# Optimization experiments

Measured on AMD Instinct MI355X. Metric: run time of the kernel, lower is better.

## Reference

```python
import jax, jax.numpy as jnp
import numpy as np

D = 4096       # embed_dim
H = 16         # num_heads
HD = D // H    # head_dim = 256
MLP_H = int(D * 2.0)  # 8192
L_V = 2048
L_T = 1024
GAMMA = 0.6
NOISE_STD = 0.07
TEMP = 0.05
LN_EPS = 1e-5


def setup_inputs() -> dict:
    key = jax.random.key(0)
    ks = jax.random.split(key, 16)
    s = 0.02
    return {
        "vision_feature": jax.random.normal(ks[0], (L_V, D), jnp.float32),
        "text_embed": jax.random.normal(ks[1], (L_T, D), jnp.float32),
        "attention_mask": jnp.zeros((L_T,), jnp.float32),  # additive mask, 0 = attend
        "noise": jax.random.normal(ks[2], (L_V,), jnp.float32),
        "Wq": jax.random.normal(ks[3], (D, D), jnp.float32) * s,
        "bq": jnp.zeros((D,), jnp.float32),
        "Wk": jax.random.normal(ks[4], (D, D), jnp.float32) * s,
        "bk": jnp.zeros((D,), jnp.float32),
        "Wv": jax.random.normal(ks[5], (D, D), jnp.float32) * s,
        "bv": jnp.zeros((D,), jnp.float32),
        "Wo": jax.random.normal(ks[6], (D, D), jnp.float32) * s,
        "bo": jnp.zeros((D,), jnp.float32),
        "ln_w": jnp.ones((D,), jnp.float32),
        "ln_b": jnp.zeros((D,), jnp.float32),
        "W1": jax.random.normal(ks[7], (MLP_H, D), jnp.float32) * s,
        "b1": jnp.zeros((MLP_H,), jnp.float32),
        "W2": jax.random.normal(ks[8], (1, MLP_H), jnp.float32) * s,
        "b2": jnp.zeros((1,), jnp.float32),
    }


def reference(vision_feature, text_embed, attention_mask, noise,
              Wq, bq, Wk, bk, Wv, bv, Wo, bo, ln_w, ln_b, W1, b1, W2, b2):
    # --- cross attention (vision queries over text keys/values) ---
    q = (vision_feature @ Wq.T + bq).reshape(L_V, H, HD)
    k = (text_embed @ Wk.T + bk).reshape(L_T, H, HD)
    v = (text_embed @ Wv.T + bv).reshape(L_T, H, HD)
    logits = jnp.einsum('qhd,khd->hqk', q, k) / np.float32(np.sqrt(HD))
    logits = logits + attention_mask[None, None, :]  # additive attn_mask
    attn = jax.nn.softmax(logits, axis=-1)
    ctx = jnp.einsum('hqk,khd->qhd', attn, v).reshape(L_V, D)
    attn_out = ctx @ Wo.T + bo
    # --- residual + layernorm ---
    x = vision_feature + attn_out
    mu = jnp.mean(x, axis=-1, keepdims=True)
    var = jnp.mean(jnp.square(x - mu), axis=-1, keepdims=True)
    xn = (x - mu) / jnp.sqrt(var + LN_EPS) * ln_w + ln_b
    # --- tiny MLP scorer ---
    h = jax.nn.gelu(xn @ W1.T + b1, approximate=False)
    weight_scores = (h @ W2.T + b2)[:, 0] + noise * NOISE_STD
    # --- temperature softmax over all tokens, top-p (gamma) selection ---
    p = jax.nn.softmax(weight_scores / TEMP, axis=0)
    order = jnp.argsort(-p)           # descending sort indices
    cum = jnp.cumsum(p[order])
    keep = cum <= GAMMA               # threshold_index prefix mask
    gathered = vision_feature[order]  # [L_V, D]
    # fixed-shape stand-in for indices[:threshold_index] gather:
    # valid selected rows are the nonzero prefix
    return jnp.where(keep[:, None], gathered, jnp.zeros((), gathered.dtype))
```

## Files before the change

### kernel.cpp

```cpp
#include <hip/hip_runtime.h>
#include <math.h>


#define LV   2048
#define LT   1024
#define DIM  4096
#define NHD  16
#define HDD  256
#define MLPH 8192

typedef __attribute__((ext_vector_type(8))) short bfx8;
typedef __attribute__((ext_vector_type(4))) float fx4;
typedef unsigned short u16;

__device__ __forceinline__ float wave_sum(float v){
#pragma unroll
  for (int o = 32; o > 0; o >>= 1) v += __shfl_xor(v, o);
  return v;
}
__device__ __forceinline__ float wave_max(float v){
#pragma unroll
  for (int o = 32; o > 0; o >>= 1) v = fmaxf(v, __shfl_xor(v, o));
  return v;
}

__device__ __forceinline__ void splitpack(const float4 a, const float4 b,
                                          bfx8* hi, bfx8* lo){
  float f[8] = {a.x,a.y,a.z,a.w, b.x,b.y,b.z,b.w};
  union { bfx8 v; unsigned u[4]; } H, L;
#pragma unroll
  for (int p = 0; p < 4; ++p){
    unsigned u0 = __float_as_uint(f[2*p]);
    unsigned u1 = __float_as_uint(f[2*p+1]);
    H.u[p] = (u0 >> 16) | (u1 & 0xffff0000u);
    float h0 = __uint_as_float(u0 & 0xffff0000u);
    float h1 = __uint_as_float(u1 & 0xffff0000u);
    unsigned v0 = __float_as_uint(f[2*p]   - h0);
    unsigned v1 = __float_as_uint(f[2*p+1] - h1);
    L.u[p] = (v0 >> 16) | (v1 & 0xffff0000u);
  }
  *hi = H.v; *lo = L.v;
}

__device__ __forceinline__ void split1(float v, u16* h, u16* l){
  unsigned uv = __float_as_uint(v);
  *h = (u16)(uv >> 16);
  float hf = __uint_as_float(uv & 0xffff0000u);
  *l = (u16)(__float_as_uint(v - hf) >> 16);
}

__device__ __forceinline__ void glds16(const void* g, void* l){
  __builtin_amdgcn_global_load_lds(
      (const __attribute__((address_space(1))) unsigned int*)g,
      (__attribute__((address_space(3))) unsigned int*)l, 16, 0, 0);
}

__global__ __launch_bounds__(256)
void repack_kernel(const float* __restrict__ src, u16* __restrict__ hi,
                   u16* __restrict__ lo, int Kc, int ktsh)
{
  const long long e = ((long long)blockIdx.x * 256 + threadIdx.x) * 8;
  const int T = (int)(e >> 9);
  const int L = (int)(e >> 3) & 63;
  const int rt = T >> ktsh, kt = T & ((1 << ktsh) - 1);
  const int r = (rt << 4) + (L & 15);
  const int k = (kt << 5) + ((L >> 4) << 3);
  const float* p = src + (long long)r * Kc + k;
  bfx8 h, l;
  splitpack(*(const float4*)p, *(const float4*)(p + 4), &h, &l);
  *(bfx8*)(hi + e) = h;
  *(bfx8*)(lo + e) = l;
}

template<int MODE>
__global__ __launch_bounds__(256)
void mgemm(const u16* __restrict__ Ah, const u16* __restrict__ Al, int aKT, long long aZe,
           const u16* __restrict__ Bh, const u16* __restrict__ Bl, int bKT, long long bZe,
           float* __restrict__ C, int ldc, long long cZe,
           u16* __restrict__ XH, u16* __restrict__ XL, int cKT, int coff0, int czoff,
           const float* __restrict__ w2, float* __restrict__ part, int nbase,
           const float* __restrict__ bias,
           int nx, int KT, int kt0, int zkt, float alpha)
{
  __shared__ bfx8 lbuf[2][32][64];
  __shared__ float parts[2][128];
  const int tid  = threadIdx.x;
  const int lane = tid & 63;
  const int wv   = tid >> 6;
  const int wr   = wv >> 1, wc = wv & 1;
  const int nwg  = gridDim.x;
  const int id   = blockIdx.x;
  int bm, bn;
  {
    const int my = nwg / nx;
    if (((nx & 3) == 0) && ((my & 1) == 0) && ((nwg & 7) == 0)){
      const int rm = my >> 1, rn = nx >> 2;
      const int x  = id & 7;
      const int j  = id >> 3;
      bm = ((x >> 2) * rm) + j / rn;
      bn = ((x & 3) * rn) + j % rn;
    } else if (((my & 7) == 0) && ((nwg & 7) == 0)){
      const int rm = my >> 3;
      const int x = id & 7, j = id >> 3;
      bm = x * rm + j / nx;
      bn = j % nx;
    } else { bm = id / nx; bn = id % nx; }
  }
  const int m0 = bm << 7;
  const int n0 = bn << 7;
  const int z    = blockIdx.z;
  const u16* Ahz = Ah + (long long)z * aZe;
  const u16* Alz = Al + (long long)z * aZe;
  const u16* Bhz = Bh + (long long)z * bZe;
  const u16* Blz = Bl + (long long)z * bZe;
  C += (long long)z * cZe;
  const int coff = coff0 + z * czoff;
  const int ktb  = kt0 + z * zkt;
  const int rtA0 = m0 >> 4, rtB0 = n0 >> 4;

  const fx4 zz = {0.f, 0.f, 0.f, 0.f};
  fx4 acc[4][4];
#pragma unroll
  for (int i = 0; i < 4; ++i)
#pragma unroll
    for (int j = 0; j < 4; ++j) acc[i][j] = zz;

  const u16* wbase = (wv == 0) ? Ahz : (wv == 1) ? Alz : (wv == 2) ? Bhz : Blz;
  const int  wrt0  = (wv < 2) ? rtA0 : rtB0;
  const int  wKT   = (wv < 2) ? aKT  : bKT;

#define STAGE(BUF, KTI)                                                        \
  {                                                                            \
    _Pragma("unroll")                                                          \
    for (int q = 0; q < 8; ++q){                                               \
      const u16* g = wbase + ((long long)(wrt0 + q) * wKT + (KTI)) * 512       \
                     + lane * 8;                                               \
      glds16((const void*)g, (void*)&lbuf[BUF][wv * 8 + q][0]);                \
    }                                                                          \
  }

#define KSTEP(WAITASM, DOSTAGE)                                                \
  {                                                                            \
    asm volatile(WAITASM ::: "memory");                                        \
    __builtin_amdgcn_sched_barrier(0);                                         \
    __builtin_amdgcn_s_barrier();                                              \
    __builtin_amdgcn_sched_barrier(0);                                         \
    bfx8 ah[4], al[4], bh[4], bl[4];                                           \
    _Pragma("unroll")                                                          \
    for (int i = 0; i < 4; ++i){                                               \
      ah[i] = lbuf[cur][     wr*4 + i][lane];                                  \
      al[i] = lbuf[cur][ 8 + wr*4 + i][lane];                                  \
      bh[i] = lbuf[cur][16 + wc*4 + i][lane];                                  \
      bl[i] = lbuf[cur][24 + wc*4 + i][lane];                                  \
    }                                                                          \
    asm volatile("s_waitcnt lgkmcnt(0)" ::: "memory");                         \
    __builtin_amdgcn_sched_barrier(0);                                         \
    __builtin_amdgcn_s_barrier();                                              \
    __builtin_amdgcn_sched_barrier(0);                                         \
    if (DOSTAGE) STAGE(cur, ktb + t + 2);                                      \
    __builtin_amdgcn_sched_barrier(0);                                         \
    _Pragma("unroll")                                                          \
    for (int i = 0; i < 4; ++i)                                                \
      _Pragma("unroll")                                                        \
      for (int j = 0; j < 4; ++j){                                             \
        acc[i][j] = __builtin_amdgcn_mfma_f32_16x16x32_bf16(ah[i], bl[j], acc[i][j], 0, 0, 0); \
        acc[i][j] = __builtin_amdgcn_mfma_f32_16x16x32_bf16(al[i], bh[j], acc[i][j], 0, 0, 0); \
        acc[i][j] = __builtin_amdgcn_mfma_f32_16x16x32_bf16(ah[i], bh[j], acc[i][j], 0, 0, 0); \
      }                                                                        \
    cur ^= 1;                                                                  \
  }

  STAGE(0, ktb);
  STAGE(1, ktb + 1);
  int cur = 0;
  for (int t = 0; t < KT - 1; ++t)
    KSTEP("s_waitcnt vmcnt(8)", (t + 2 < KT));
  { const int t = KT - 1; (void)t; KSTEP("s_waitcnt vmcnt(0)", 0); }
#undef KSTEP
#undef STAGE

  if (MODE == 0){
#pragma unroll
    for (int i = 0; i < 4; ++i){
      const int row0 = m0 + wr*64 + i*16 + ((lane >> 4) << 2);
#pragma unroll
      for (int j = 0; j < 4; ++j){
        const int col = n0 + wc*64 + j*16 + (lane & 15);
        const float bb = bias ? bias[col] : 0.0f;
#pragma unroll
        for (int r = 0; r < 4; ++r)
          C[(size_t)(row0 + r)*ldc + col] = alpha*acc[i][j][r] + bb;
      }
    }
  } else if (MODE == 2){
#pragma unroll
    for (int i = 0; i < 4; ++i){
      const int row0 = m0 + wr*64 + i*16 + ((lane >> 4) << 2);
#pragma unroll
      for (int j = 0; j < 4; ++j){
        const int ncol = n0 + wc*64 + j*16 + (lane & 15);
        const int colg = coff + ncol;
        const float bb = bias ? bias[ncol] : 0.0f;
        const long long base = (long long)(row0 >> 4) * cKT + (colg >> 5);
        const int el = colg & 7;
        const int sl0 = ((colg >> 3) & 3) * 16 + (row0 & 15);
        u16* ph = XH + base*512 + el;
        u16* pl = XL + base*512 + el;
#pragma unroll
        for (int r = 0; r < 4; ++r){
          u16 hh, llo;
          split1(alpha*acc[i][j][r] + bb, &hh, &llo);
          ph[(sl0 + r)*8] = hh;
          pl[(sl0 + r)*8] = llo;
        }
      }
    }
  } else if (MODE == 3){
#pragma unroll
    for (int i = 0; i < 4; ++i){
      const int row0 = m0 + wr*64 + i*16 + ((lane >> 4) << 2);
#pragma unroll
      for (int j = 0; j < 4; ++j){
        const int d = n0 + wc*64 + j*16 + (lane & 15);
        const float bb = bias ? bias[d] : 0.0f;
        short4 hs, ls;
        u16 h0,l0,h1,l1,h2,l2,h3,l3;
        split1(alpha*acc[i][j][0] + bb, &h0, &l0);
        split1(alpha*acc[i][j][1] + bb, &h1, &l1);
        split1(alpha*acc[i][j][2] + bb, &h2, &l2);
        split1(alpha*acc[i][j][3] + bb, &h3, &l3);
        hs.x=(short)h0; hs.y=(short)h1; hs.z=(short)h2; hs.w=(short)h3;
        ls.x=(short)l0; ls.y=(short)l1; ls.z=(short)l2; ls.w=(short)l3;
        const long long T = (long long)(d >> 4) * cKT + (row0 >> 5);
        const int sl = ((row0 >> 3) & 3) * 16 + (d & 15);
        *(short4*)(XH + T*512 + sl*8 + (row0 & 7)) = hs;
        *(short4*)(XL + T*512 + sl*8 + (row0 & 7)) = ls;
      }
    }
  } else if (MODE == 4){
    float rp[16];
#pragma unroll
    for (int q = 0; q < 16; ++q) rp[q] = 0.0f;
#pragma unroll
    for (int i = 0; i < 4; ++i){
#pragma unroll
      for (int j = 0; j < 4; ++j){
        const int ncol = n0 + wc*64 + j*16 + (lane & 15);
        const float bb = bias[ncol];
        const float ww = w2[ncol];
#pragma unroll
        for (int r = 0; r < 4; ++r){
          float v = alpha*acc[i][j][r] + bb;
          v = 0.5f*v*(1.0f + erff(v*0.70710678f));
          rp[i*4 + r] += v * ww;
        }
      }
    }
#pragma unroll
    for (int mK = 1; mK <= 8; mK <<= 1)
#pragma unroll
      for (int q = 0; q < 16; ++q) rp[q] += __shfl_xor(rp[q], mK);
    if ((lane & 15) == 0){
#pragma unroll
      for (int q = 0; q < 16; ++q){
        const int i = q >> 2, r = q & 3;
        parts[wc][wr*64 + i*16 + ((lane >> 4) << 2) + r] = rp[q];
      }
    }
    __syncthreads();
    if (tid < 128)
      part[(long long)(m0 + tid)*64 + nbase + (n0 >> 7)] =
          parts[0][tid] + parts[1][tid];
  }
}

template<int GELU, int TRANSC>
__global__ __launch_bounds__(256)
void mgemm_fb(const float* __restrict__ A, long long aZ, int lda,
              const float* __restrict__ B, long long bZ, int ldb,
              float* __restrict__ C, long long cZ, int ldc,
              const float* __restrict__ bias, int Kd, float alpha)
{
  __shared__ bfx8 AhS[512], AlS[512], BhS[512], BlS[512];
  const int tid  = threadIdx.x;
  const int lane = tid & 63;
  const int wv   = tid >> 6;
  const int wr   = wv >> 1, wc = wv & 1;
  const int m0 = blockIdx.y * 128, n0 = blockIdx.x * 128;
  A += (long long)blockIdx.z * aZ;
  B += (long long)blockIdx.z * bZ;
  C += (long long)blockIdx.z * cZ;

  const fx4 zz = {0.f, 0.f, 0.f, 0.f};
  fx4 acc[4][4];
#pragma unroll
  for (int i = 0; i < 4; ++i)
#pragma unroll
    for (int j = 0; j < 4; ++j) acc[i][j] = zz;

  for (int k0 = 0; k0 < Kd; k0 += 32){
    __syncthreads();
#pragma unroll
    for (int pass = 0; pass < 2; ++pass){
      const int s = pass*256 + tid;
      const int m = ((s >> 6) << 4) + (s & 15);
      const int j = (s >> 4) & 3;
      const float* pA = A + (size_t)(m0 + m)*lda + k0 + j*8;
      splitpack(*(const float4*)pA, *(const float4*)(pA + 4), &AhS[s], &AlS[s]);
      const float* pB = B + (size_t)(n0 + m)*ldb + k0 + j*8;
      splitpack(*(const float4*)pB, *(const float4*)(pB + 4), &BhS[s], &BlS[s]);
    }
    __syncthreads();
    bfx8 ah[4], al[4], bh[4], bl[4];
#pragma unroll
    for (int i = 0; i < 4; ++i){
      ah[i] = AhS[(wr*4 + i)*64 + lane];
      al[i] = AlS[(wr*4 + i)*64 + lane];
      bh[i] = BhS[(wc*4 + i)*64 + lane];
      bl[i] = BlS[(wc*4 + i)*64 + lane];
    }
#pragma unroll
    for (int i = 0; i < 4; ++i)
#pragma unroll
      for (int j = 0; j < 4; ++j){
        acc[i][j] = __builtin_amdgcn_mfma_f32_16x16x32_bf16(ah[i], bl[j], acc[i][j], 0, 0, 0);
        acc[i][j] = __builtin_amdgcn_mfma_f32_16x16x32_bf16(al[i], bh[j], acc[i][j], 0, 0, 0);
        acc[i][j] = __builtin_amdgcn_mfma_f32_16x16x32_bf16(ah[i], bh[j], acc[i][j], 0, 0, 0);
      }
  }
#pragma unroll
  for (int i = 0; i < 4; ++i){
    const int row0 = m0 + wr*64 + i*16 + ((lane >> 4) << 2);
#pragma unroll
    for (int j = 0; j < 4; ++j){
      const int col = n0 + wc*64 + j*16 + (lane & 15);
      const float bb = bias ? bias[col] : 0.0f;
      if (TRANSC){
        float4 o;
        o.x = alpha*acc[i][j][0] + bb;
        o.y = alpha*acc[i][j][1] + bb;
        o.z = alpha*acc[i][j][2] + bb;
        o.w = alpha*acc[i][j][3] + bb;
        *(float4*)(C + (size_t)col*ldc + row0) = o;
      } else {
#pragma unroll
        for (int r = 0; r < 4; ++r){
          float v = alpha*acc[i][j][r] + bb;
          if (GELU) v = 0.5f*v*(1.0f + erff(v*0.70710678f));
          C[(size_t)(row0 + r)*ldc + col] = v;
        }
      }
    }
  }
}

__global__ __launch_bounds__(128)
void softmax_pack(const float* __restrict__ Lf, u16* __restrict__ ph,
                  u16* __restrict__ pl)
{
  __shared__ float rr[4];
  const int tid = threadIdx.x;
  const int h = blockIdx.x >> 11;
  const int m = blockIdx.x & 2047;
  const float* row = Lf + ((long long)h * 2048 + m) * 1024;
  const int k = tid * 8;
  float4 a = *(const float4*)(row + k);
  float4 b = *(const float4*)(row + k + 4);
  float v[8] = {a.x,a.y,a.z,a.w, b.x,b.y,b.z,b.w};
  float mx = v[0];
#pragma unroll
  for (int i = 1; i < 8; ++i) mx = fmaxf(mx, v[i]);
  mx = wave_max(mx);
  if ((tid & 63) == 0) rr[tid >> 6] = mx;
  __syncthreads();
  const float M = fmaxf(rr[0], rr[1]);
  float e[8], s = 0.0f;
#pragma unroll
  for (int i = 0; i < 8; ++i){ e[i] = expf(v[i] - M); s += e[i]; }
  s = wave_sum(s);
  if ((tid & 63) == 0) rr[2 + (tid >> 6)] = s;
  __syncthreads();
  const float S = rr[2] + rr[3];
  float4 p0 = make_float4(e[0]/S, e[1]/S, e[2]/S, e[3]/S);
  float4 p1 = make_float4(e[4]/S, e[5]/S, e[6]/S, e[7]/S);
  bfx8 hh, ll;
  splitpack(p0, p1, &hh, &ll);
  const int tile = (m >> 4) * 32 + (k >> 5);
  const int Lw = ((k >> 3) & 3) * 16 + (m & 15);
  const long long eoff = (long long)h * (2048ll*1024) + (long long)tile * 512 + Lw * 8;
  *(bfx8*)(ph + eoff) = hh;
  *(bfx8*)(pl + eoff) = ll;
}

__global__ __launch_bounds__(256)
void softmax_fb(float* __restrict__ X)
{
  __shared__ float r[8];
  const int tid = threadIdx.x;
  float* row = X + (size_t)blockIdx.x * 1024;
  float4 v = ((const float4*)row)[tid];
  float m = fmaxf(fmaxf(v.x,v.y), fmaxf(v.z,v.w));
  m = wave_max(m);
  if ((tid & 63) == 0) r[tid >> 6] = m;
  __syncthreads();
  m = fmaxf(fmaxf(r[0],r[1]), fmaxf(r[2],r[3]));
  float e0 = expf(v.x - m), e1 = expf(v.y - m), e2 = expf(v.z - m), e3 = expf(v.w - m);
  float s = (e0 + e1) + (e2 + e3);
  s = wave_sum(s);
  if ((tid & 63) == 0) r[4 + (tid >> 6)] = s;
  __syncthreads();
  s = (r[4] + r[5]) + (r[6] + r[7]);
  ((float4*)row)[tid] = make_float4(e0/s, e1/s, e2/s, e3/s);
}

template<int PACK>
__global__ __launch_bounds__(256)
void ln_kernel(const float* __restrict__ vis, const float* ao, float* xnf,
               u16* __restrict__ xh, u16* __restrict__ xl,
               const float* __restrict__ w, const float* __restrict__ b)
{
  __shared__ float r[8];
  __shared__ float stat[2];
  const int tid = threadIdx.x;
  const int m = blockIdx.x;
  const size_t base = (size_t)m * DIM + tid * 16;
  float x[16];
#pragma unroll
  for (int q = 0; q < 4; ++q){
    float4 a = *(const float4*)(vis + base + q*4);
    float4 c = *(const float4*)(ao  + base + q*4);
    x[q*4+0]=a.x+c.x; x[q*4+1]=a.y+c.y; x[q*4+2]=a.z+c.z; x[q*4+3]=a.w+c.w;
  }
  float s = 0.0f;
#pragma unroll
  for (int i = 0; i < 16; ++i) s += x[i];
  s = wave_sum(s);
  if ((tid & 63) == 0) r[tid >> 6] = s;
  __syncthreads();
  if (tid == 0) stat[0] = (r[0]+r[1]+r[2]+r[3]) * (1.0f/4096.0f);
  __syncthreads();
  const float mu = stat[0];
  float vs = 0.0f;
#pragma unroll
  for (int i = 0; i < 16; ++i){ float d = x[i]-mu; vs += d*d; }
  vs = wave_sum(vs);
  if ((tid & 63) == 0) r[4 + (tid >> 6)] = vs;
  __syncthreads();
  if (tid == 0) stat[1] = (r[4]+r[5]+r[6]+r[7]) * (1.0f/4096.0f);
  __syncthreads();
  const float inv = 1.0f / sqrtf(stat[1] + 1e-5f);
  const int col = tid * 16;
  float o[16];
#pragma unroll
  for (int q = 0; q < 4; ++q){
    float4 wv = *(const float4*)(w + col + q*4);
    float4 bv = *(const float4*)(b + col + q*4);
    o[q*4+0] = (x[q*4+0]-mu)*inv*wv.x + bv.x;
    o[q*4+1] = (x[q*4+1]-mu)*inv*wv.y + bv.y;
    o[q*4+2] = (x[q*4+2]-mu)*inv*wv.z + bv.z;
    o[q*4+3] = (x[q*4+3]-mu)*inv*wv.w + bv.w;
  }
  if (PACK){
#pragma unroll
    for (int q = 0; q < 2; ++q){
      const int k = col + q*8;
      float4 p0 = make_float4(o[q*8+0], o[q*8+1], o[q*8+2], o[q*8+3]);
      float4 p1 = make_float4(o[q*8+4], o[q*8+5], o[q*8+6], o[q*8+7]);
      bfx8 hh, ll;
      splitpack(p0, p1, &hh, &ll);
      const int tile = (m >> 4) * 128 + (k >> 5);
      const int Lw = ((k >> 3) & 3) * 16 + (m & 15);
      const long long e = (long long)tile * 512 + Lw * 8;
      *(bfx8*)(xh + e) = hh;
      *(bfx8*)(xl + e) = ll;
    }
  } else {
#pragma unroll
    for (int q = 0; q < 4; ++q)
      *(float4*)(xnf + base + q*4) = make_float4(o[q*4+0],o[q*4+1],o[q*4+2],o[q*4+3]);
  }
}

__global__ __launch_bounds__(64)
void score_reduce(const float* __restrict__ part, const float* __restrict__ b2,
                  const float* __restrict__ noise, float* __restrict__ sc)
{
  const int row = blockIdx.x;
  float s = part[(long long)row*64 + threadIdx.x];
  s = wave_sum(s);
  if (threadIdx.x == 0) sc[row] = s + b2[0] + noise[row]*0.07f;
}

__global__ __launch_bounds__(256)
void score_kernel(const float* __restrict__ H1, const float* __restrict__ W2v,
                  const float* __restrict__ b2, const float* __restrict__ noise,
                  float* __restrict__ sc)
{
  __shared__ float r[4];
  const int tid = threadIdx.x;
  const float* h = H1 + (size_t)blockIdx.x * MLPH + tid * 32;
  const float* w = W2v + tid * 32;
  float s = 0.0f;
#pragma unroll
  for (int q = 0; q < 8; ++q){
    float4 a = *(const float4*)(h + q*4);
    float4 c = *(const float4*)(w + q*4);
    s += a.x*c.x + a.y*c.y + a.z*c.z + a.w*c.w;
  }
  s = wave_sum(s);
  if ((tid & 63) == 0) r[tid >> 6] = s;
  __syncthreads();
  if (tid == 0) sc[blockIdx.x] = (r[0]+r[1]+r[2]+r[3]) + b2[0] + noise[blockIdx.x]*0.07f;
}

__global__ __launch_bounds__(1024)
void select_kernel(const float* __restrict__ scores,
                   int* __restrict__ ord, int* __restrict__ kcount)
{
  __shared__ float sv[LV];
  __shared__ int   si[LV];
  __shared__ float red[32];
  __shared__ float stat[2];
  const int tid = threadIdx.x;
  for (int i = tid; i < LV; i += 1024){ sv[i] = scores[i] / 0.05f; si[i] = i; }
  __syncthreads();
  float m = -3.4e38f;
  for (int i = tid; i < LV; i += 1024) m = fmaxf(m, sv[i]);
  m = wave_max(m);
  if ((tid & 63) == 0) red[tid >> 6] = m;
  __syncthreads();
  if (tid == 0){
    float M = red[0];
    for (int w = 1; w < 16; ++w) M = fmaxf(M, red[w]);
    stat[0] = M;
  }
  __syncthreads();
  const float ymax = stat[0];
  float d = 0.0f;
  for (int i = tid; i < LV; i += 1024) d += expf(sv[i] - ymax);
  d = wave_sum(d);
  if ((tid & 63) == 0) red[16 + (tid >> 6)] = d;
  __syncthreads();
  if (tid == 0){
    float D = 0.0f;
    for (int w = 0; w < 16; ++w) D += red[16 + w];
    stat[1] = D;
  }
  __syncthreads();
  const float denom = stat[1];
  for (int size = 2; size <= LV; size <<= 1){
    for (int stride = size >> 1; stride > 0; stride >>= 1){
      __syncthreads();
      const int i = 2*tid - (tid & (stride - 1));
      const int j = i + stride;
      const bool up = ((i & size) == 0);
      float a = sv[i], b = sv[j];
      if ((a < b) == up){
        sv[i] = b; sv[j] = a;
        int ti = si[i]; si[i] = si[j]; si[j] = ti;
      }
    }
  }
  __syncthreads();
  for (int i = tid; i < LV; i += 1024) sv[i] = expf(sv[i] - ymax) / denom;
  __syncthreads();
  if (tid == 0){
    float c = 0.0f; int kc = LV;
    for (int j = 0; j < LV; ++j){
      c += sv[j];
      if (!((double)c <= 0.6)){ kc = j; break; }
    }
    *kcount = kc;
  }
  __syncthreads();
  for (int i = tid; i < LV; i += 1024) ord[i] = si[i];
}

__global__ __launch_bounds__(256)
void writer_kernel(const float* __restrict__ vis, const int* __restrict__ ord,
                   const int* __restrict__ kc, float* __restrict__ out)
{
  const int j = blockIdx.x;
  float4* dst = (float4*)(out + (size_t)j * DIM);
  if (j < kc[0]){
    const float4* src = (const float4*)(vis + (size_t)ord[j] * DIM);
    for (int i = threadIdx.x; i < DIM/4; i += 256) dst[i] = src[i];
  } else {
    const float4 z4 = make_float4(0.f,0.f,0.f,0.f);
    for (int i = threadIdx.x; i < DIM/4; i += 256) dst[i] = z4;
  }
}

extern "C" void kernel_launch(void* const* d_in, const int* in_sizes, int n_in,
                              void* d_out, int out_size, void* d_ws, size_t ws_size,
                              hipStream_t stream)
{
  (void)in_sizes; (void)n_in; (void)out_size;
  const float* vis  = (const float*)d_in[0];
  const float* txt  = (const float*)d_in[1];
  const float* mask = (const float*)d_in[2];
  const float* noise= (const float*)d_in[3];
  const float* Wq = (const float*)d_in[4];  const float* bq = (const float*)d_in[5];
  const float* Wk = (const float*)d_in[6];  const float* bk = (const float*)d_in[7];
  const float* Wv = (const float*)d_in[8];  const float* bv = (const float*)d_in[9];
  const float* Wo = (const float*)d_in[10]; const float* bo = (const float*)d_in[11];
  const float* lw = (const float*)d_in[12]; const float* lb = (const float*)d_in[13];
  const float* W1 = (const float*)d_in[14]; const float* b1 = (const float*)d_in[15];
  const float* W2 = (const float*)d_in[16]; const float* b2 = (const float*)d_in[17];
  float* out = (float*)d_out;
  const dim3 blk(256);
  const size_t MiB = 1u << 20;

  int Hc = 0;
  for (int h = 16; h >= 1; h >>= 1){
    size_t need = (177 + 16 * (size_t)h) * MiB;
    if (need <= ws_size){ Hc = h; break; }
  }

  if (Hc > 0){
    char* B0 = (char*)d_ws;
    u16* WSh  = (u16*)(B0 + 0);          u16* WSl  = (u16*)(B0 + 32*MiB);
    u16* VCh  = (u16*)(B0 + 64*MiB);     u16* VCl  = (u16*)(B0 + 80*MiB);
    u16* TCh  = (u16*)(B0 + 96*MiB);     u16* TCl  = (u16*)(B0 + 104*MiB);
    u16* QCh  = (u16*)(B0 + 112*MiB);    u16* QCl  = (u16*)(B0 + 128*MiB);
    u16* KCh  = (u16*)(B0 + 144*MiB);    u16* KCl  = (u16*)(B0 + 152*MiB);
    u16* VTCh = (u16*)(B0 + 160*MiB);    u16* VTCl = (u16*)(B0 + 168*MiB);
    float* TMPf = (float*)(B0 + 144*MiB);
    u16* XNh  = (u16*)(B0 + 112*MiB);    u16* XNl  = (u16*)(B0 + 128*MiB);
    float* Lf  = (float*)(B0 + 176*MiB);
    u16* PCh  = (u16*)(B0 + (176 + (size_t)Hc*8)*MiB);
    u16* PCl  = (u16*)(B0 + (176 + (size_t)Hc*12)*MiB);
    float* PART = (float*)(B0 + 176*MiB);
    float* SCf  = (float*)(B0 + 176*MiB + 524288);
    int* ORD = (int*)(SCf + LV);
    int* KCp = ORD + LV;

    repack_kernel<<<dim3(4096), blk, 0, stream>>>(vis, VCh, VCl, 4096, 7);
    repack_kernel<<<dim3(2048), blk, 0, stream>>>(txt, TCh, TCl, 4096, 7);
    repack_kernel<<<dim3(8192), blk, 0, stream>>>(Wq, WSh, WSl, 4096, 7);
    mgemm<2><<<dim3(512,1,1), blk, 0, stream>>>(VCh, VCl, 128, 0, WSh, WSl, 128, 0,
        nullptr, 0, 0, QCh, QCl, 128, 0, 0, nullptr, nullptr, 0, bq, 32, 128, 0, 0, 1.0f);
    repack_kernel<<<dim3(8192), blk, 0, stream>>>(Wk, WSh, WSl, 4096, 7);
    mgemm<2><<<dim3(256,1,1), blk, 0, stream>>>(TCh, TCl, 128, 0, WSh, WSl, 128, 0,
        nullptr, 0, 0, KCh, KCl, 128, 0, 0, nullptr, nullptr, 0, bk, 32, 128, 0, 0, 1.0f);
    repack_kernel<<<dim3(8192), blk, 0, stream>>>(Wv, WSh, WSl, 4096, 7);
    mgemm<3><<<dim3(256,1,1), blk, 0, stream>>>(TCh, TCl, 128, 0, WSh, WSl, 128, 0,
        nullptr, 0, 0, VTCh, VTCl, 32, 0, 0, nullptr, nullptr, 0, bv, 32, 128, 0, 0, 1.0f);
    const int NG = NHD / Hc;
    for (int g = 0; g < NG; ++g){
      mgemm<0><<<dim3(128,1,Hc), blk, 0, stream>>>(QCh, QCl, 128, 0, KCh, KCl, 128, 0,
          Lf, 1024, 2097152ll, nullptr, nullptr, 0, 0, 0, nullptr, nullptr, 0,
          mask, 8, 8, g*Hc*8, 8, 0.0625f);
      softmax_pack<<<dim3(Hc*2048), dim3(128), 0, stream>>>(Lf, PCh, PCl);
      mgemm<2><<<dim3(32,1,Hc), blk, 0, stream>>>(PCh, PCl, 32, 2097152ll,
          VTCh + (long long)g*Hc*262144, VTCl + (long long)g*Hc*262144, 32, 262144ll,
          nullptr, 0, 0, VCh, VCl, 128, g*Hc*256, 256, nullptr, nullptr, 0,
          nullptr, 2, 32, 0, 0, 1.0f);
    }
    repack_kernel<<<dim3(8192), blk, 0, stream>>>(Wo, WSh, WSl, 4096, 7);
    mgemm<0><<<dim3(512,1,1), blk, 0, stream>>>(VCh, VCl, 128, 0, WSh, WSl, 128, 0,
        TMPf, 4096, 0, nullptr, nullptr, 0, 0, 0, nullptr, nullptr, 0,
        bo, 32, 128, 0, 0, 1.0f);
    ln_kernel<1><<<dim3(LV), blk, 0, stream>>>(vis, TMPf, nullptr, XNh, XNl, lw, lb);
    repack_kernel<<<dim3(8192), blk, 0, stream>>>(W1, WSh, WSl, 4096, 7);
    mgemm<4><<<dim3(512,1,1), blk, 0, stream>>>(XNh, XNl, 128, 0, WSh, WSl, 128, 0,
        nullptr, 0, 0, nullptr, nullptr, 0, 0, 0, W2, PART, 0,
        b1, 32, 128, 0, 0, 1.0f);
    repack_kernel<<<dim3(8192), blk, 0, stream>>>(W1 + 16777216ll, WSh, WSl, 4096, 7);
    mgemm<4><<<dim3(512,1,1), blk, 0, stream>>>(XNh, XNl, 128, 0, WSh, WSl, 128, 0,
        nullptr, 0, 0, nullptr, nullptr, 0, 0, 0, W2 + 4096, PART, 32,
        b1 + 4096, 32, 128, 0, 0, 1.0f);
    score_reduce<<<dim3(LV), dim3(64), 0, stream>>>(PART, b2, noise, SCf);
    select_kernel<<<dim3(1), dim3(1024), 0, stream>>>(SCf, ORD, KCp);
    writer_kernel<<<dim3(LV), blk, 0, stream>>>(vis, ORD, KCp, out);
    return;
  }

  float* ws = (float*)d_ws;
  const long long OQ  = 0;
  const long long OK_ = (long long)LV * DIM;
  const long long OV  = OK_ + (long long)LT * DIM;
  const long long OC  = OV  + (long long)LT * DIM;
  const long long OL  = OC  + (long long)LV * DIM;
  const long long LSTRIDE = (long long)LV * LT;
  int Hf = 16;
  while (Hf > 1){
    size_t need = (size_t)(OL + (long long)Hf * LSTRIDE + 8192) * 4;
    if (need <= ws_size) break;
    Hf >>= 1;
  }
  float* Qw  = ws + OQ;
  float* Kw  = ws + OK_;
  float* Vt  = ws + OV;
  float* Cw  = ws + OC;
  float* Lw  = ws + OL;
  float* H1w = ws + OK_;
  float* SCw = ws + OL + (long long)Hf * LSTRIDE;
  int*   ORDw = (int*)(SCw + LV);
  int*   KCw  = ORDw + LV;

  mgemm_fb<0,0><<<dim3(DIM/128, LV/128, 1), blk, 0, stream>>>(vis,0,DIM, Wq,0,DIM, Qw,0,DIM, bq, DIM, 1.0f);
  mgemm_fb<0,0><<<dim3(DIM/128, LT/128, 1), blk, 0, stream>>>(txt,0,DIM, Wk,0,DIM, Kw,0,DIM, bk, DIM, 1.0f);
  mgemm_fb<0,1><<<dim3(DIM/128, LT/128, 1), blk, 0, stream>>>(txt,0,DIM, Wv,0,DIM, Vt,0,LT, bv, DIM, 1.0f);
  for (int g = 0; g < NHD/Hf; ++g){
    const long long ho = (long long)g * Hf * HDD;
    mgemm_fb<0,0><<<dim3(LT/128, LV/128, Hf), blk, 0, stream>>>(
        Qw+ho, HDD, DIM,  Kw+ho, HDD, DIM,  Lw, LSTRIDE, LT,  mask, HDD, 0.0625f);
    softmax_fb<<<dim3(Hf*LV), blk, 0, stream>>>(Lw);
    mgemm_fb<0,0><<<dim3(HDD/128, LV/128, Hf), blk, 0, stream>>>(
        Lw, LSTRIDE, LT,  Vt + (ho*(long long)LT), (long long)HDD*LT, LT,
        Cw+ho, HDD, DIM,  nullptr, LT, 1.0f);
  }
  mgemm_fb<0,0><<<dim3(DIM/128, LV/128, 1), blk, 0, stream>>>(Cw,0,DIM, Wo,0,DIM, Qw,0,DIM, bo, DIM, 1.0f);
  ln_kernel<0><<<dim3(LV), blk, 0, stream>>>(vis, Qw, Qw, nullptr, nullptr, lw, lb);
  mgemm_fb<1,0><<<dim3(MLPH/128, LV/128, 1), blk, 0, stream>>>(Qw,0,DIM, W1,0,DIM, H1w,0,MLPH, b1, DIM, 1.0f);
  score_kernel<<<dim3(LV), blk, 0, stream>>>(H1w, W2, b2, noise, SCw);
  select_kernel<<<dim3(1), dim3(1024), 0, stream>>>(SCw, ORDw, KCw);
  writer_kernel<<<dim3(LV), blk, 0, stream>>>(vis, ORDw, KCw, out);
}
```

Before: 1.487 ms.

## Replace two-deep async GEMM pipeline with single-barrier double buffering

Replaces the hand-tuned main loop of the split-bf16 MFMA GEMM with a plain double-buffered loop. The old loop prefetched two K-tiles ahead and used explicit vmcnt/lgkmcnt waits with two barriers per step. The new loop has one __syncthreads per step and prefetches only one tile ahead. The per-block reduction scratch for the fused GELU-scorer epilogue now reuses the staging LDS buffer behind an extra barrier, which trims shared memory. The cost is less latency hiding, since the barrier likely drains all outstanding global loads on every iteration.

```diff
diff --git a/kernel.cpp b/kernel.cpp
--- a/kernel.cpp
+++ b/kernel.cpp
@@ -83,7 +83,6 @@
            int nx, int KT, int kt0, int zkt, float alpha)
 {
   __shared__ bfx8 lbuf[2][32][64];
-  __shared__ float parts[2][128];
   const int tid  = threadIdx.x;
   const int lane = tid & 63;
   const int wv   = tid >> 6;
@@ -139,44 +138,29 @@
     }                                                                          \
   }
 
-#define KSTEP(WAITASM, DOSTAGE)                                                \
-  {                                                                            \
-    asm volatile(WAITASM ::: "memory");                                        \
-    __builtin_amdgcn_sched_barrier(0);                                         \
-    __builtin_amdgcn_s_barrier();                                              \
-    __builtin_amdgcn_sched_barrier(0);                                         \
-    bfx8 ah[4], al[4], bh[4], bl[4];                                           \
-    _Pragma("unroll")                                                          \
-    for (int i = 0; i < 4; ++i){                                               \
-      ah[i] = lbuf[cur][     wr*4 + i][lane];                                  \
-      al[i] = lbuf[cur][ 8 + wr*4 + i][lane];                                  \
-      bh[i] = lbuf[cur][16 + wc*4 + i][lane];                                  \
-      bl[i] = lbuf[cur][24 + wc*4 + i][lane];                                  \
-    }                                                                          \
-    asm volatile("s_waitcnt lgkmcnt(0)" ::: "memory");                         \
-    __builtin_amdgcn_sched_barrier(0);                                         \
-    __builtin_amdgcn_s_barrier();                                              \
-    __builtin_amdgcn_sched_barrier(0);                                         \
-    if (DOSTAGE) STAGE(cur, ktb + t + 2);                                      \
-    __builtin_amdgcn_sched_barrier(0);                                         \
-    _Pragma("unroll")                                                          \
-    for (int i = 0; i < 4; ++i)                                                \
-      _Pragma("unroll")                                                        \
-      for (int j = 0; j < 4; ++j){                                             \
-        acc[i][j] = __builtin_amdgcn_mfma_f32_16x16x32_bf16(ah[i], bl[j], acc[i][j], 0, 0, 0); \
-        acc[i][j] = __builtin_amdgcn_mfma_f32_16x16x32_bf16(al[i], bh[j], acc[i][j], 0, 0, 0); \
-        acc[i][j] = __builtin_amdgcn_mfma_f32_16x16x32_bf16(ah[i], bh[j], acc[i][j], 0, 0, 0); \
-      }                                                                        \
-    cur ^= 1;                                                                  \
-  }
-
+  int cur = 0;
   STAGE(0, ktb);
-  STAGE(1, ktb + 1);
-  int cur = 0;
-  for (int t = 0; t < KT - 1; ++t)
-    KSTEP("s_waitcnt vmcnt(8)", (t + 2 < KT));
-  { const int t = KT - 1; (void)t; KSTEP("s_waitcnt vmcnt(0)", 0); }
-#undef KSTEP
+  for (int t = 0; t < KT; ++t){
+    __syncthreads();
+    if (t + 1 < KT) STAGE(cur ^ 1, ktb + t + 1);
+    bfx8 ah[4], al[4], bh[4], bl[4];
+#pragma unroll
+    for (int i = 0; i < 4; ++i){
+      ah[i] = lbuf[cur][     wr*4 + i][lane];
+      al[i] = lbuf[cur][ 8 + wr*4 + i][lane];
+      bh[i] = lbuf[cur][16 + wc*4 + i][lane];
+      bl[i] = lbuf[cur][24 + wc*4 + i][lane];
+    }
+#pragma unroll
+    for (int i = 0; i < 4; ++i)
+#pragma unroll
+      for (int j = 0; j < 4; ++j){
+        acc[i][j] = __builtin_amdgcn_mfma_f32_16x16x32_bf16(ah[i], bl[j], acc[i][j], 0, 0, 0);
+        acc[i][j] = __builtin_amdgcn_mfma_f32_16x16x32_bf16(al[i], bh[j], acc[i][j], 0, 0, 0);
+        acc[i][j] = __builtin_amdgcn_mfma_f32_16x16x32_bf16(ah[i], bh[j], acc[i][j], 0, 0, 0);
+      }
+    cur ^= 1;
+  }
 #undef STAGE
 
   if (MODE == 0){
@@ -260,17 +244,19 @@
     for (int mK = 1; mK <= 8; mK <<= 1)
 #pragma unroll
       for (int q = 0; q < 16; ++q) rp[q] += __shfl_xor(rp[q], mK);
+    float* partsf = (float*)&lbuf[0][0][0];
+    __syncthreads();
     if ((lane & 15) == 0){
 #pragma unroll
       for (int q = 0; q < 16; ++q){
         const int i = q >> 2, r = q & 3;
-        parts[wc][wr*64 + i*16 + ((lane >> 4) << 2) + r] = rp[q];
+        partsf[wc*128 + wr*64 + i*16 + ((lane >> 4) << 2) + r] = rp[q];
       }
     }
     __syncthreads();
     if (tid < 128)
       part[(long long)(m0 + tid)*64 + nbase + (n0 >> 7)] =
-          parts[0][tid] + parts[1][tid];
+          partsf[tid] + partsf[128 + tid];
   }
 }
 
```

Result: slower. 1.535 ms (+3.2%).
